# Optimization experiments

Measured on AMD Instinct MI355X. Metric: run time of the kernel, lower is better.

## Reference

```python
import jax, jax.numpy as jnp
import numpy as np

H, DK, D, DFF = 8, 64, 512, 512
B, S = 4, 1024
SCALE = 1.0 / np.sqrt(DK)


def _ln(x, g, b, eps=1e-5):
    m = jnp.mean(x, axis=-1, keepdims=True)
    v = jnp.mean((x - m) ** 2, axis=-1, keepdims=True)
    return (x - m) / jnp.sqrt(v + eps) * g + b


def _heads(x, w, b):
    bs, s, _ = x.shape
    return (x @ w + b).reshape(bs, s, H, DK).transpose(0, 2, 1, 3)  # [B,H,S,DK]


def _encoder_layer(x, qw, qb, kw, kb, vw, vb, ow, ob, g1, b1, w1, c1, w2, c2, g2, b2):
    # standard post-LN transformer encoder layer (sub_attention.Encoder(1))
    q = _heads(x, qw, qb)
    k = _heads(x, kw, kb)
    v = _heads(x, vw, vb)
    attn = jax.nn.softmax(jnp.einsum('bhqd,bhkd->bhqk', q, k) * SCALE, axis=-1)
    ctx = jnp.einsum('bhqk,bhkd->bhqd', attn, v).transpose(0, 2, 1, 3).reshape(x.shape[0], -1, H * DK)
    h = _ln(ctx @ ow + ob + x, g1, b1)
    f = jax.nn.relu(h @ w1 + c1) @ w2 + c2
    return _ln(f + h, g2, b2)


def setup_inputs() -> dict:
    key = jax.random.key(0)
    ks = iter(jax.random.split(key, 80))

    def nrm(*shape):
        return jax.random.normal(next(ks), shape, jnp.float32) * 0.02

    inp = {'audio_feat': jax.random.normal(next(ks), (B, S, D), jnp.float32),
           'video_feat': jax.random.normal(next(ks), (B, S, D), jnp.float32)}
    for p in ['aq', 'ak', 'av', 'vq', 'vk', 'vv', 'out']:
        inp[p + '_w'] = nrm(D, D)
        inp[p + '_b'] = jnp.zeros((D,), jnp.float32)
    inp['ln_g'] = jnp.ones((D,), jnp.float32)
    inp['ln_b'] = jnp.zeros((D,), jnp.float32)
    for pfx in ['asa_', 'vsa_']:
        for wn in ['qw', 'kw', 'vw', 'ow']:
            inp[pfx + wn] = nrm(D, D)
        for bn in ['qb', 'kb', 'vb', 'ob']:
            inp[pfx + bn] = jnp.zeros((D,), jnp.float32)
        inp[pfx + 'w1'] = nrm(D, DFF)
        inp[pfx + 'c1'] = jnp.zeros((DFF,), jnp.float32)
        inp[pfx + 'w2'] = nrm(DFF, D)
        inp[pfx + 'c2'] = jnp.zeros((D,), jnp.float32)
        inp[pfx + 'g1'] = jnp.ones((D,), jnp.float32)
        inp[pfx + 'b1'] = jnp.zeros((D,), jnp.float32)
        inp[pfx + 'g2'] = jnp.ones((D,), jnp.float32)
        inp[pfx + 'b2'] = jnp.zeros((D,), jnp.float32)
    return inp


def reference(audio_feat, video_feat, aq_w, aq_b, ak_w, ak_b, av_w, av_b, vq_w, vq_b, vk_w, vk_b, vv_w, vv_b, out_w, out_b, ln_g, ln_b, asa_qw, asa_qb, asa_kw, asa_kb, asa_vw, asa_vb, asa_ow, asa_ob, asa_g1, asa_b1, asa_w1, asa_c1, asa_w2, asa_c2, asa_g2, asa_b2, vsa_qw, vsa_qb, vsa_kw, vsa_kb, vsa_vw, vsa_vb, vsa_ow, vsa_ob, vsa_g1, vsa_b1, vsa_w1, vsa_c1, vsa_w2, vsa_c2, vsa_g2, vsa_b2):
    audio_self = _encoder_layer(audio_feat, asa_qw, asa_qb, asa_kw, asa_kb, asa_vw, asa_vb, asa_ow, asa_ob, asa_g1, asa_b1, asa_w1, asa_c1, asa_w2, asa_c2, asa_g2, asa_b2)
    video_self = _encoder_layer(video_feat, vsa_qw, vsa_qb, vsa_kw, vsa_kb, vsa_vw, vsa_vb, vsa_ow, vsa_ob, vsa_g1, vsa_b1, vsa_w1, vsa_c1, vsa_w2, vsa_c2, vsa_g2, vsa_b2)
    qa = _heads(audio_feat, aq_w, aq_b)
    ka = _heads(audio_feat, ak_w, ak_b)
    va = _heads(audio_feat, av_w, av_b)
    qv = _heads(video_feat, vq_w, vq_b)
    kv = _heads(video_feat, vk_w, vk_b)
    vvh = _heads(video_feat, vv_w, vv_b)
    attn_a = jax.nn.softmax(jnp.einsum('bhqd,bhkd->bhqk', qa, ka) * SCALE, axis=-1)
    attn_v = jax.nn.softmax(jnp.einsum('bhqd,bhkd->bhqk', qv, kv) * SCALE, axis=-1)
    attn = attn_a * attn_v  # dual-softmax elementwise combine
    ctx = jnp.einsum('bhqk,bhkd->bhqd', attn, va) * jnp.einsum('bhqk,bhkd->bhqd', attn, vvh)
    ctx = ctx.transpose(0, 2, 1, 3).reshape(audio_feat.shape[0], -1, H * DK)
    context = ctx @ out_w + out_b
    return _ln(audio_feat + context + audio_self + video_self, ln_g, ln_b)
```

## Files before the change

kernel.cpp:

```cpp
#include <hip/hip_runtime.h>
#include <cstddef>
#include <cstdint>


typedef __attribute__((ext_vector_type(8))) short s8v;
typedef __attribute__((ext_vector_type(4))) short s4v;
typedef __attribute__((ext_vector_type(4))) float f4v;

#define QSC 0.1803368801111444f
#define EXP2(x) __builtin_amdgcn_exp2f(x)
#define WAITV(N) asm volatile("s_waitcnt vmcnt(" #N ")" ::: "memory")
#define BAR() __builtin_amdgcn_s_barrier()

static __device__ __forceinline__ short f2bf(float f){
  unsigned int u = __builtin_bit_cast(unsigned int, f);
  u += 0x7fffu + ((u >> 16) & 1u);
  return (short)(u >> 16);
}
static __device__ __forceinline__ float bf2f(short s){
  unsigned int u = ((unsigned int)(unsigned short)s) << 16;
  return __builtin_bit_cast(float, u);
}
static __device__ __forceinline__ void gload16(const void* g, void* l){
  __builtin_amdgcn_global_load_lds(
      (const __attribute__((address_space(1))) unsigned int*)g,
      (__attribute__((address_space(3))) unsigned int*)l, 16, 0, 0);
}
#define MFMA16(a,b,c) __builtin_amdgcn_mfma_f32_16x16x32_bf16(a,b,c,0,0,0)

__global__ __launch_bounds__(256) void convert_in(const float* __restrict__ a,
                                                  const float* __restrict__ v,
                                                  short* __restrict__ oa,
                                                  short* __restrict__ ov){
  const float* src = blockIdx.y ? v : a;
  short* dst = blockIdx.y ? ov : oa;
  const int i = (blockIdx.x * 256 + threadIdx.x) * 8;
  float4 x = *reinterpret_cast<const float4*>(src + i);
  float4 y = *reinterpret_cast<const float4*>(src + i + 4);
  s8v o;
  o[0]=f2bf(x.x); o[1]=f2bf(x.y); o[2]=f2bf(x.z); o[3]=f2bf(x.w);
  o[4]=f2bf(y.x); o[5]=f2bf(y.y); o[6]=f2bf(y.z); o[7]=f2bf(y.w);
  *reinterpret_cast<s8v*>(dst + i) = o;
}

struct Ptr19 { const float* p[19]; };
__global__ __launch_bounds__(256) void pack_w(Ptr19 ws, short* __restrict__ wp){
  const int mat = blockIdx.y;
  const float* W = ws.p[mat];
  const int f = blockIdx.x * 256 + threadIdx.x;
  const int nblk = f >> 10, kg = (f >> 4) & 63, nl = f & 15;
  const int n = nblk * 16 + nl, k = kg * 8;
  s8v o;
#pragma unroll
  for (int e = 0; e < 8; ++e) o[e] = f2bf(W[(size_t)(k + e) * 512 + n]);
  *reinterpret_cast<s8v*>(wp + (size_t)mat * 262144 + (size_t)f * 8) = o;
}

struct GemmJobs { const short* A[12]; const short* W[12]; const float* bias[12];
                  short* C[12]; int mode[12]; };

template<bool RELU>
__global__ __launch_bounds__(256) void gemm_bf16(GemmJobs J){
  int i = (blockIdx.z * 32 + blockIdx.y) * 4 + blockIdx.x;
  const int c = (128 * gridDim.z) >> 3;
  i = (i & 7) * c + (i >> 3);
  const int z = i >> 7, rem = i & 127;
  const int by = rem >> 2, bx = rem & 3;

  const short* __restrict__ A = J.A[z];
  const short* __restrict__ Wp = J.W[z];
  const float* __restrict__ bias = J.bias[z];
  short* __restrict__ C = J.C[z];
  const int md = J.mode[z];
  __shared__ short As[2][4096], Bs[2][4096];
  const int tid = threadIdx.x, lane = tid & 63, w = tid >> 6;
  const int wm = w >> 1, wn = w & 1;
  const int m0 = by * 128, n0 = bx * 128;
  const int lh = lane >> 4, ll = lane & 15;
  f4v acc[4][4] = {};

  auto stage = [&](int kt, int buf){
    const int k0 = kt * 32;
#pragma unroll
    for (int p = 0; p < 2; ++p){
      const int f = tid + 256 * p;
      const int blk = f >> 6, kg = (f >> 4) & 3, il = f & 15;
      gload16(A + (size_t)(m0 + blk * 16 + il) * 512 + k0 + kg * 8, &As[buf][f * 8]);
      gload16(Wp + ((size_t)(((n0 >> 4) + blk) * 64 + (k0 >> 3) + kg) * 16 + il) * 8,
              &Bs[buf][f * 8]);
    }
  };

  stage(0, 0);
#pragma unroll
  for (int kt = 0; kt < 16; ++kt){
    if (kt < 15) { stage(kt + 1, (kt + 1) & 1); WAITV(4); }
    else         { WAITV(0); }
    BAR();
    const int cur = kt & 1;
    s8v a[4], b[4];
#pragma unroll
    for (int q = 0; q < 4; ++q)
      a[q] = *reinterpret_cast<const s8v*>(&As[cur][(((wm*4+q)*4 + lh)*16 + ll) * 8]);
#pragma unroll
    for (int j = 0; j < 4; ++j)
      b[j] = *reinterpret_cast<const s8v*>(&Bs[cur][(((wn*4+j)*4 + lh)*16 + ll) * 8]);
#pragma unroll
    for (int q = 0; q < 4; ++q)
#pragma unroll
      for (int j = 0; j < 4; ++j)
        acc[q][j] = MFMA16(a[q], b[j], acc[q][j]);
    BAR();
  }

  if (md == 2){
#pragma unroll
    for (int j = 0; j < 4; ++j){
      const int col = n0 + wn * 64 + j * 16 + ll;
      const float bv = bias[col];
      const int hh = col >> 6, dl = col & 63, dblk = dl >> 4, il = dl & 15;
#pragma unroll
      for (int q = 0; q < 4; ++q){
        const int rowb = m0 + wm * 64 + q * 16 + lh * 4;
        const int bb = rowb >> 10, srow = rowb & 1023;
        const size_t off = ((size_t)((bb*8 + hh)*16 + (srow >> 6))) * 4096
                         + (size_t)(((dblk << 7) + (((srow >> 3) & 7) << 4) + il) * 8 + (srow & 7));
        s4v o4;
#pragma unroll
        for (int r = 0; r < 4; ++r) o4[r] = f2bf(acc[q][j][r] + bv);
        *reinterpret_cast<s4v*>(&C[off]) = o4;
      }
    }
  } else {
    short* epi = (w < 2) ? &As[w][0] : &Bs[w - 2][0];
    const float sc = (md == 1) ? QSC : 1.0f;
#pragma unroll
    for (int j = 0; j < 4; ++j){
      const float bv = bias[n0 + wn * 64 + j * 16 + ll];
#pragma unroll
      for (int q = 0; q < 4; ++q)
#pragma unroll
        for (int r = 0; r < 4; ++r){
          float v = (acc[q][j][r] + bv) * sc;
          if (RELU) v = fmaxf(v, 0.f);
          epi[(q*16 + lh*4 + r)*64 + j*16 + ll] = f2bf(v);
        }
    }
#pragma unroll
    for (int i2 = 0; i2 < 8; ++i2){
      const int row = i2 * 8 + (lane >> 3);
      s8v vr = *reinterpret_cast<const s8v*>(&epi[row*64 + (lane & 7)*8]);
      *reinterpret_cast<s8v*>(&C[(size_t)(m0 + wm*64 + row)*512 + n0 + wn*64 + (lane&7)*8]) = vr;
    }
  }
}

template<bool RELU>
__global__ __launch_bounds__(256) void gemm_n64(GemmJobs J){
  int i = (blockIdx.z * 32 + blockIdx.y) * 8 + blockIdx.x;
  const int c = (256 * gridDim.z) >> 3;
  i = (i & 7) * c + (i >> 3);
  const int z = i >> 8, rem = i & 255;
  const int by = rem >> 3, bx = rem & 7;

  const short* __restrict__ A = J.A[z];
  const short* __restrict__ Wp = J.W[z];
  const float* __restrict__ bias = J.bias[z];
  short* __restrict__ C = J.C[z];
  __shared__ short As[2][4096], Bs[2][2048];
  const int tid = threadIdx.x, lane = tid & 63, w = tid >> 6;
  const int wm = w >> 1, wn = w & 1;
  const int m0 = by * 128, n0 = bx * 64;
  const int lh = lane >> 4, ll = lane & 15;
  f4v acc[4][2] = {};

  auto stage = [&](int kt, int buf){
    const int k0 = kt * 32;
#pragma unroll
    for (int p = 0; p < 2; ++p){
      const int f = tid + 256 * p;
      const int blk = f >> 6, kg = (f >> 4) & 3, il = f & 15;
      gload16(A + (size_t)(m0 + blk * 16 + il) * 512 + k0 + kg * 8, &As[buf][f * 8]);
    }
    {
      const int f = tid;
      const int blk = f >> 6, kg = (f >> 4) & 3, il = f & 15;
      gload16(Wp + ((size_t)(((n0 >> 4) + blk) * 64 + (k0 >> 3) + kg) * 16 + il) * 8,
              &Bs[buf][f * 8]);
    }
  };

  stage(0, 0);
#pragma unroll
  for (int kt = 0; kt < 16; ++kt){
    if (kt < 15) { stage(kt + 1, (kt + 1) & 1); WAITV(3); }
    else         { WAITV(0); }
    BAR();
    const int cur = kt & 1;
    s8v a[4], b[2];
#pragma unroll
    for (int q = 0; q < 4; ++q)
      a[q] = *reinterpret_cast<const s8v*>(&As[cur][(((wm*4+q)*4 + lh)*16 + ll) * 8]);
#pragma unroll
    for (int j = 0; j < 2; ++j)
      b[j] = *reinterpret_cast<const s8v*>(&Bs[cur][(((wn*2+j)*4 + lh)*16 + ll) * 8]);
#pragma unroll
    for (int q = 0; q < 4; ++q)
#pragma unroll
      for (int j = 0; j < 2; ++j)
        acc[q][j] = MFMA16(a[q], b[j], acc[q][j]);
    BAR();
  }

  short* epi = &As[0][0] + w * 2048;
#pragma unroll
  for (int j = 0; j < 2; ++j){
    const float bv = bias[n0 + wn * 32 + j * 16 + ll];
#pragma unroll
    for (int q = 0; q < 4; ++q)
#pragma unroll
      for (int r = 0; r < 4; ++r){
        float v = acc[q][j][r] + bv;
        if (RELU) v = fmaxf(v, 0.f);
        epi[(q*16 + lh*4 + r)*32 + j*16 + ll] = f2bf(v);
      }
  }
#pragma unroll
  for (int i2 = 0; i2 < 4; ++i2){
    const int row = i2 * 16 + (lane >> 2);
    s8v vr = *reinterpret_cast<const s8v*>(&epi[row*32 + (lane & 3)*8]);
    *reinterpret_cast<s8v*>(&C[(size_t)(m0 + wm*64 + row)*512 + n0 + wn*32 + (lane&3)*8]) = vr;
  }
}

struct AttnJob { const short* Q; const short* K; const short* Vp; short* O; };

__global__ __launch_bounds__(512) void attn_enc(AttnJob j0, AttnJob j1){
  const AttnJob jb = blockIdx.z ? j1 : j0;
  __shared__ short KT[2][4096], VT[2][4096];
  __shared__ short PL[8][1024];
  const int tid = threadIdx.x, lane = tid & 63, w = tid >> 6;
  int bi = blockIdx.y * 8 + blockIdx.x;
  bi = (bi & 7) * 32 + (bi >> 3);
  const int qt = bi & 7, bh = bi >> 3;
  const int b = bh >> 3, h = bh & 7;
  const int q0 = qt * 128;
  const size_t base = (size_t)b * 1024 * 512 + (size_t)h * 64;
  const int lh = lane >> 4, ll = lane & 15;
  short* PLw = PL[w];

  s8v qf[2];
#pragma unroll
  for (int df = 0; df < 2; ++df)
    qf[df] = *reinterpret_cast<const s8v*>(jb.Q + base + (size_t)(q0 + w*16 + ll)*512 + lh*8 + df*32);

  const int sblk = tid >> 7, sg8 = (tid >> 4) & 7, sil = tid & 15;
  auto stage = [&](int it, int buf){
    gload16(jb.K + base + (size_t)(it*64 + sblk*16 + sil)*512 + sg8*8, &KT[buf][tid*8]);
    gload16(jb.Vp + ((size_t)bh*16 + it)*4096 + (size_t)tid*8, &VT[buf][tid*8]);
  };

  f4v o[4] = {};
  float lp[4] = {0.f, 0.f, 0.f, 0.f};

  stage(0, 0);
#pragma unroll 1
  for (int it = 0; it < 16; ++it){
    if (it < 15) { stage(it + 1, (it + 1) & 1); WAITV(2); }
    else         { WAITV(0); }
    BAR();
    const int cur = it & 1;

    f4v s[4] = {};
#pragma unroll
    for (int fn = 0; fn < 4; ++fn)
#pragma unroll
      for (int df = 0; df < 2; ++df){
        s8v kf = *reinterpret_cast<const s8v*>(&KT[cur][((fn*8 + lh + df*4)*16 + ll) * 8]);
        s[fn] = MFMA16(qf[df], kf, s[fn]);
      }

    float px[4][4];
#pragma unroll
    for (int r = 0; r < 4; ++r){
      float p0 = EXP2(s[0][r]), p1 = EXP2(s[1][r]);
      float p2 = EXP2(s[2][r]), p3 = EXP2(s[3][r]);
      px[r][0]=p0; px[r][1]=p1; px[r][2]=p2; px[r][3]=p3;
      lp[r] += (p0 + p1) + (p2 + p3);
    }
#pragma unroll
    for (int r = 0; r < 4; ++r)
#pragma unroll
      for (int fn = 0; fn < 4; ++fn){
        const int q = lh*4 + r, k = fn*16 + ll, kg = k >> 3;
        PLw[(kg*16 + (q ^ kg))*8 + (k & 7)] = f2bf(px[r][fn]);
      }
    s8v pa[2];
#pragma unroll
    for (int kf2 = 0; kf2 < 2; ++kf2){
      const int kg = lh + kf2*4;
      pa[kf2] = *reinterpret_cast<const s8v*>(&PLw[(kg*16 + (ll ^ kg))*8]);
    }
#pragma unroll
    for (int fd = 0; fd < 4; ++fd)
#pragma unroll
      for (int kf2 = 0; kf2 < 2; ++kf2){
        s8v vf = *reinterpret_cast<const s8v*>(&VT[cur][((fd*8 + lh + kf2*4)*16 + ll) * 8]);
        o[fd] = MFMA16(pa[kf2], vf, o[fd]);
      }
    BAR();
  }

#pragma unroll
  for (int r = 0; r < 4; ++r){
    float Z = lp[r];
    Z += __shfl_xor(Z, 1); Z += __shfl_xor(Z, 2);
    Z += __shfl_xor(Z, 4); Z += __shfl_xor(Z, 8);
    const float rz = 1.f / Z;
#pragma unroll
    for (int fd = 0; fd < 4; ++fd)
      jb.O[base + (size_t)(q0 + w*16 + lh*4 + r)*512 + fd*16 + ll] = f2bf(o[fd][r] * rz);
  }
}

__global__ __launch_bounds__(512) void attn_dual(const short* __restrict__ Qa, const short* __restrict__ Ka,
                                                 const short* __restrict__ Vap, const short* __restrict__ Qv,
                                                 const short* __restrict__ Kv, const short* __restrict__ Vvp,
                                                 short* __restrict__ O){
  __shared__ short KTa[2][4096], KTv[2][4096], VTa[2][4096], VTv[2][4096];
  __shared__ short PL[8][1024];
  const int tid = threadIdx.x, lane = tid & 63, w = tid >> 6;
  int bi = blockIdx.y * 8 + blockIdx.x;
  bi = (bi & 7) * 32 + (bi >> 3);
  const int qt = bi & 7, bh = bi >> 3;
  const int b = bh >> 3, h = bh & 7;
  const int q0 = qt * 128;
  const size_t base = (size_t)b * 1024 * 512 + (size_t)h * 64;
  const int lh = lane >> 4, ll = lane & 15;
  short* PLw = PL[w];

  s8v qfa[2], qfv[2];
#pragma unroll
  for (int df = 0; df < 2; ++df){
    const size_t ro = base + (size_t)(q0 + w*16 + ll)*512 + lh*8 + df*32;
    qfa[df] = *reinterpret_cast<const s8v*>(Qa + ro);
    qfv[df] = *reinterpret_cast<const s8v*>(Qv + ro);
  }

  const int sblk = tid >> 7, sg8 = (tid >> 4) & 7, sil = tid & 15;
  auto stage = [&](int it, int buf){
    const size_t krow = base + (size_t)(it*64 + sblk*16 + sil)*512 + sg8*8;
    gload16(Ka + krow, &KTa[buf][tid*8]);
    gload16(Kv + krow, &KTv[buf][tid*8]);
    const size_t voff = ((size_t)bh*16 + it)*4096 + (size_t)tid*8;
    gload16(Vap + voff, &VTa[buf][tid*8]);
    gload16(Vvp + voff, &VTv[buf][tid*8]);
  };

  f4v oa[4] = {}, ov[4] = {};
  float lap[4] = {0,0,0,0}, lvp[4] = {0,0,0,0};

  stage(0, 0);
#pragma unroll 1
  for (int it = 0; it < 16; ++it){
    if (it < 15) { stage(it + 1, (it + 1) & 1); WAITV(4); }
    else         { WAITV(0); }
    BAR();
    const int cur = it & 1;

    f4v sa[4] = {}, sv[4] = {};
#pragma unroll
    for (int fn = 0; fn < 4; ++fn)
#pragma unroll
      for (int df = 0; df < 2; ++df){
        const int boff = ((fn*8 + lh + df*4)*16 + ll) * 8;
        s8v ka = *reinterpret_cast<const s8v*>(&KTa[cur][boff]);
        s8v kv = *reinterpret_cast<const s8v*>(&KTv[cur][boff]);
        sa[fn] = MFMA16(qfa[df], ka, sa[fn]);
        sv[fn] = MFMA16(qfv[df], kv, sv[fn]);
      }

    float pt[4][4];
#pragma unroll
    for (int r = 0; r < 4; ++r){
      float a0 = EXP2(sa[0][r]), a1 = EXP2(sa[1][r]);
      float a2 = EXP2(sa[2][r]), a3 = EXP2(sa[3][r]);
      float v0 = EXP2(sv[0][r]), v1 = EXP2(sv[1][r]);
      float v2 = EXP2(sv[2][r]), v3 = EXP2(sv[3][r]);
      lap[r] += (a0 + a1) + (a2 + a3);
      lvp[r] += (v0 + v1) + (v2 + v3);
      pt[r][0] = a0*v0; pt[r][1] = a1*v1; pt[r][2] = a2*v2; pt[r][3] = a3*v3;
    }
#pragma unroll
    for (int r = 0; r < 4; ++r)
#pragma unroll
      for (int fn = 0; fn < 4; ++fn){
        const int q = lh*4 + r, k = fn*16 + ll, kg = k >> 3;
        PLw[(kg*16 + (q ^ kg))*8 + (k & 7)] = f2bf(pt[r][fn]);
      }
    s8v pa[2];
#pragma unroll
    for (int kf2 = 0; kf2 < 2; ++kf2){
      const int kg = lh + kf2*4;
      pa[kf2] = *reinterpret_cast<const s8v*>(&PLw[(kg*16 + (ll ^ kg))*8]);
    }
#pragma unroll
    for (int fd = 0; fd < 4; ++fd)
#pragma unroll
      for (int kf2 = 0; kf2 < 2; ++kf2){
        const int boff = ((fd*8 + lh + kf2*4)*16 + ll) * 8;
        s8v va = *reinterpret_cast<const s8v*>(&VTa[cur][boff]);
        s8v vv = *reinterpret_cast<const s8v*>(&VTv[cur][boff]);
        oa[fd] = MFMA16(pa[kf2], va, oa[fd]);
        ov[fd] = MFMA16(pa[kf2], vv, ov[fd]);
      }
    BAR();
  }

#pragma unroll
  for (int r = 0; r < 4; ++r){
    float Za = lap[r], Zv = lvp[r];
    Za += __shfl_xor(Za, 1); Za += __shfl_xor(Za, 2);
    Za += __shfl_xor(Za, 4); Za += __shfl_xor(Za, 8);
    Zv += __shfl_xor(Zv, 1); Zv += __shfl_xor(Zv, 2);
    Zv += __shfl_xor(Zv, 4); Zv += __shfl_xor(Zv, 8);
    const float rz = 1.f / (Za * Zv);
#pragma unroll
    for (int fd = 0; fd < 4; ++fd){
      const float v = (oa[fd][r] * rz) * (ov[fd][r] * rz);
      O[base + (size_t)(q0 + w*16 + lh*4 + r)*512 + fd*16 + ll] = f2bf(v);
    }
  }
}

struct LnJob { const short* xb0; const short* xb1; const short* xb2;
               const float* xf; const float* g; const float* bb; void* out; };

template<int NBF, bool ADDF32, bool OUTF32>
__global__ __launch_bounds__(256) void ln_fused(LnJob j0, LnJob j1){
  const LnJob j = blockIdx.y ? j1 : j0;
  const int row = blockIdx.x, t = threadIdx.x;
  const size_t base = (size_t)row * 512;
  float x[2];
#pragma unroll
  for (int u = 0; u < 2; ++u){
    const int c = t + u * 256;
    float v = bf2f(j.xb0[base + c]);
    if (NBF > 1) v += bf2f(j.xb1[base + c]);
    if (NBF > 2) v += bf2f(j.xb2[base + c]);
    if (ADDF32) v += j.xf[base + c];
    x[u] = v;
  }
  float s = x[0] + x[1], ss = x[0]*x[0] + x[1]*x[1];
#pragma unroll
  for (int o = 32; o; o >>= 1){ s += __shfl_xor(s, o); ss += __shfl_xor(ss, o); }
  __shared__ float rb[8];
  const int wv = t >> 6;
  if ((t & 63) == 0){ rb[wv] = s; rb[wv + 4] = ss; }
  __syncthreads();
  s  = rb[0] + rb[1] + rb[2] + rb[3];
  ss = rb[4] + rb[5] + rb[6] + rb[7];
  const float m = s * (1.f / 512.f);
  const float var = ss * (1.f / 512.f) - m * m;
  const float rstd = rsqrtf(var + 1e-5f);
#pragma unroll
  for (int u = 0; u < 2; ++u){
    const int c = t + u * 256;
    const float v = (x[u] - m) * rstd * j.g[c] + j.bb[c];
    if (OUTF32) ((float*)j.out)[base + c] = v;
    else        ((short*)j.out)[base + c] = f2bf(v);
  }
}

__global__ __launch_bounds__(256) void ln_final(const short* __restrict__ fa, const short* __restrict__ ha,
                                                const short* __restrict__ fv, const short* __restrict__ hv,
                                                const short* __restrict__ ctx, const float* __restrict__ audio,
                                                const float* __restrict__ g2a, const float* __restrict__ b2a,
                                                const float* __restrict__ g2v, const float* __restrict__ b2v,
                                                const float* __restrict__ gf, const float* __restrict__ bf,
                                                float* __restrict__ out){
  const int row = blockIdx.x, t = threadIdx.x;
  const size_t base = (size_t)row * 512;
  __shared__ float rb[24];
  const int wv = t >> 6;

  auto reduce2 = [&](float a, float b, int p){
    float s = a + b, ss = a*a + b*b;
#pragma unroll
    for (int o = 32; o; o >>= 1){ s += __shfl_xor(s, o); ss += __shfl_xor(ss, o); }
    if ((t & 63) == 0){ rb[p*8 + wv] = s; rb[p*8 + 4 + wv] = ss; }
  };
  auto stats = [&](int p, float& m, float& rstd){
    const float s  = rb[p*8+0] + rb[p*8+1] + rb[p*8+2] + rb[p*8+3];
    const float ss = rb[p*8+4] + rb[p*8+5] + rb[p*8+6] + rb[p*8+7];
    m = s * (1.f / 512.f);
    rstd = rsqrtf(ss * (1.f / 512.f) - m * m + 1e-5f);
  };

  float xa[2], xv[2];
#pragma unroll
  for (int u = 0; u < 2; ++u){
    const int c = t + u * 256;
    xa[u] = bf2f(fa[base + c]) + bf2f(ha[base + c]);
    xv[u] = bf2f(fv[base + c]) + bf2f(hv[base + c]);
  }
  reduce2(xa[0], xa[1], 0);
  reduce2(xv[0], xv[1], 1);
  __syncthreads();
  float ma, ra, mv, rv;
  stats(0, ma, ra);
  stats(1, mv, rv);

  float xf[2];
#pragma unroll
  for (int u = 0; u < 2; ++u){
    const int c = t + u * 256;
    const float sa = (xa[u] - ma) * ra * g2a[c] + b2a[c];
    const float sv = (xv[u] - mv) * rv * g2v[c] + b2v[c];
    xf[u] = audio[base + c] + bf2f(ctx[base + c]) + sa + sv;
  }
  reduce2(xf[0], xf[1], 2);
  __syncthreads();
  float mf, rf;
  stats(2, mf, rf);
#pragma unroll
  for (int u = 0; u < 2; ++u){
    const int c = t + u * 256;
    out[base + c] = (xf[u] - mf) * rf * gf[c] + bf[c];
  }
}

extern "C" void kernel_launch(void* const* d_in, const int* in_sizes, int n_in,
                              void* d_out, int out_size, void* d_ws, size_t ws_size,
                              hipStream_t stream) {
  const float* audio = (const float*)d_in[0];
  const float* video = (const float*)d_in[1];
  auto F = [&](int i){ return (const float*)d_in[i]; };

  short* ws16 = (short*)d_ws;
  const size_t SL = 2097152;
  auto S = [&](int i){ return ws16 + (size_t)i * SL; };
  short* Wp = S(12);
  auto WP = [&](int i){ return (const short*)(Wp + (size_t)i * 262144); };
  short* Kcv = (short*)d_out;
  short* Vcv = (short*)d_out + SL;

  convert_in<<<dim3(1024,2), 256, 0, stream>>>(audio, video, S(10), S(11));

  Ptr19 pw;
  const int widx[19] = {18,19,20,21,26,28, 34,35,36,37,42,44, 2,4,6,8,10,12, 14};
  for (int i = 0; i < 19; ++i) pw.p[i] = F(widx[i]);
  pack_w<<<dim3(128,19), 256, 0, stream>>>(pw, Wp);

  GemmJobs g1{};
  const short* g1A[12] = {S(10),S(10),S(10), S(11),S(11),S(11), S(10),S(10),S(10), S(11),S(11),S(11)};
  const short* g1W[12] = {WP(0),WP(1),WP(2), WP(6),WP(7),WP(8), WP(12),WP(13),WP(14), WP(15),WP(16),WP(17)};
  const float* g1B[12] = {F(22),F(23),F(24), F(38),F(39),F(40), F(3),F(5),F(7), F(9),F(11),F(13)};
  short*       g1C[12] = {S(0),S(1),S(2), S(3),S(4),S(5), S(6),S(7),S(8), S(9),Kcv,Vcv};
  const int    g1M[12] = {1,0,2, 1,0,2, 1,0,2, 1,0,2};
  for (int i = 0; i < 12; ++i){ g1.A[i]=g1A[i]; g1.W[i]=g1W[i]; g1.bias[i]=g1B[i]; g1.C[i]=g1C[i]; g1.mode[i]=g1M[i]; }
  gemm_bf16<false><<<dim3(4,32,12), 256, 0, stream>>>(g1);

  attn_enc<<<dim3(8,32,2), 512, 0, stream>>>(AttnJob{S(0),S(1),S(2),S(10)},
                                             AttnJob{S(3),S(4),S(5),S(11)});

  attn_dual<<<dim3(8,32), 512, 0, stream>>>(S(6),S(7),S(8), S(9),Kcv,Vcv, S(0));

  GemmJobs g39{};
  g39.A[0]=S(10); g39.W[0]=WP(3);  g39.bias[0]=F(25); g39.C[0]=S(1); g39.mode[0]=0;
  g39.A[1]=S(11); g39.W[1]=WP(9);  g39.bias[1]=F(41); g39.C[1]=S(2); g39.mode[1]=0;
  g39.A[2]=S(0);  g39.W[2]=WP(18); g39.bias[2]=F(15); g39.C[2]=S(3); g39.mode[2]=0;
  gemm_n64<false><<<dim3(8,32,3), 256, 0, stream>>>(g39);

  ln_fused<1,true,false><<<dim3(4096,2), 256, 0, stream>>>(
      LnJob{S(1),nullptr,nullptr, audio, F(30),F(31), S(4)},
      LnJob{S(2),nullptr,nullptr, video, F(46),F(47), S(5)});

  GemmJobs g5{};
  g5.A[0]=S(4); g5.W[0]=WP(4);  g5.bias[0]=F(27); g5.C[0]=S(6); g5.mode[0]=0;
  g5.A[1]=S(5); g5.W[1]=WP(10); g5.bias[1]=F(43); g5.C[1]=S(7); g5.mode[1]=0;
  gemm_n64<true><<<dim3(8,32,2), 256, 0, stream>>>(g5);

  GemmJobs g6{};
  g6.A[0]=S(6); g6.W[0]=WP(5);  g6.bias[0]=F(29); g6.C[0]=S(8); g6.mode[0]=0;
  g6.A[1]=S(7); g6.W[1]=WP(11); g6.bias[1]=F(45); g6.C[1]=S(9); g6.mode[1]=0;
  gemm_n64<false><<<dim3(8,32,2), 256, 0, stream>>>(g6);

  ln_final<<<4096, 256, 0, stream>>>(S(8),S(4), S(9),S(5), S(3), audio,
                                     F(32),F(33), F(48),F(49), F(16),F(17),
                                     (float*)d_out);
}
```

Baseline: 183.0 us.

## Halve attention block threads so each wave computes two query tiles

Both attention kernels now run 4 waves per block instead of 8. Each wave handles 32 query rows as two 16-row tiles, so every K and V fragment read from shared memory feeds two MFMAs. Staging is split into two load passes per thread and the vmcnt waits are doubled to match. The aim is fewer LDS reads per MFMA and cheaper barriers, at the cost of higher register pressure and fewer waves available to hide latency.

```diff
diff --git a/kernel.cpp b/kernel.cpp
--- a/kernel.cpp
+++ b/kernel.cpp
@@ -235,10 +235,10 @@
 
 struct AttnJob { const short* Q; const short* K; const short* Vp; short* O; };
 
-__global__ __launch_bounds__(512) void attn_enc(AttnJob j0, AttnJob j1){
+__global__ __launch_bounds__(256) void attn_enc(AttnJob j0, AttnJob j1){
   const AttnJob jb = blockIdx.z ? j1 : j0;
   __shared__ short KT[2][4096], VT[2][4096];
-  __shared__ short PL[8][1024];
+  __shared__ short PL[4][2048];
   const int tid = threadIdx.x, lane = tid & 63, w = tid >> 6;
   int bi = blockIdx.y * 8 + blockIdx.x;
   bi = (bi & 7) * 32 + (bi >> 3);
@@ -247,88 +247,107 @@
   const int q0 = qt * 128;
   const size_t base = (size_t)b * 1024 * 512 + (size_t)h * 64;
   const int lh = lane >> 4, ll = lane & 15;
-  short* PLw = PL[w];
-
-  s8v qf[2];
-#pragma unroll
-  for (int df = 0; df < 2; ++df)
-    qf[df] = *reinterpret_cast<const s8v*>(jb.Q + base + (size_t)(q0 + w*16 + ll)*512 + lh*8 + df*32);
-
-  const int sblk = tid >> 7, sg8 = (tid >> 4) & 7, sil = tid & 15;
+
+  s8v qf[2][2];
+#pragma unroll
+  for (int t = 0; t < 2; ++t)
+#pragma unroll
+    for (int df = 0; df < 2; ++df)
+      qf[t][df] = *reinterpret_cast<const s8v*>(
+          jb.Q + base + (size_t)(q0 + w*32 + t*16 + ll)*512 + lh*8 + df*32);
+
   auto stage = [&](int it, int buf){
-    gload16(jb.K + base + (size_t)(it*64 + sblk*16 + sil)*512 + sg8*8, &KT[buf][tid*8]);
-    gload16(jb.Vp + ((size_t)bh*16 + it)*4096 + (size_t)tid*8, &VT[buf][tid*8]);
+#pragma unroll
+    for (int p = 0; p < 2; ++p){
+      const int f = tid + 256 * p;
+      const int sblk = f >> 7, sg8 = (f >> 4) & 7, sil = f & 15;
+      gload16(jb.K + base + (size_t)(it*64 + sblk*16 + sil)*512 + sg8*8, &KT[buf][f*8]);
+      gload16(jb.Vp + ((size_t)bh*16 + it)*4096 + (size_t)f*8, &VT[buf][f*8]);
+    }
   };
 
-  f4v o[4] = {};
-  float lp[4] = {0.f, 0.f, 0.f, 0.f};
+  f4v o[2][4] = {};
+  float lp[2][4] = {};
 
   stage(0, 0);
 #pragma unroll 1
   for (int it = 0; it < 16; ++it){
-    if (it < 15) { stage(it + 1, (it + 1) & 1); WAITV(2); }
+    if (it < 15) { stage(it + 1, (it + 1) & 1); WAITV(4); }
     else         { WAITV(0); }
     BAR();
     const int cur = it & 1;
 
-    f4v s[4] = {};
+    f4v s[2][4] = {};
 #pragma unroll
     for (int fn = 0; fn < 4; ++fn)
 #pragma unroll
       for (int df = 0; df < 2; ++df){
         s8v kf = *reinterpret_cast<const s8v*>(&KT[cur][((fn*8 + lh + df*4)*16 + ll) * 8]);
-        s[fn] = MFMA16(qf[df], kf, s[fn]);
-      }
-
-    float px[4][4];
-#pragma unroll
-    for (int r = 0; r < 4; ++r){
-      float p0 = EXP2(s[0][r]), p1 = EXP2(s[1][r]);
-      float p2 = EXP2(s[2][r]), p3 = EXP2(s[3][r]);
-      px[r][0]=p0; px[r][1]=p1; px[r][2]=p2; px[r][3]=p3;
-      lp[r] += (p0 + p1) + (p2 + p3);
-    }
-#pragma unroll
-    for (int r = 0; r < 4; ++r)
-#pragma unroll
-      for (int fn = 0; fn < 4; ++fn){
-        const int q = lh*4 + r, k = fn*16 + ll, kg = k >> 3;
-        PLw[(kg*16 + (q ^ kg))*8 + (k & 7)] = f2bf(px[r][fn]);
-      }
-    s8v pa[2];
-#pragma unroll
-    for (int kf2 = 0; kf2 < 2; ++kf2){
-      const int kg = lh + kf2*4;
-      pa[kf2] = *reinterpret_cast<const s8v*>(&PLw[(kg*16 + (ll ^ kg))*8]);
-    }
+#pragma unroll
+        for (int t = 0; t < 2; ++t)
+          s[t][fn] = MFMA16(qf[t][df], kf, s[t][fn]);
+      }
+
+#pragma unroll
+    for (int t = 0; t < 2; ++t){
+      short* PLt = &PL[w][t*1024];
+      float px[4][4];
+#pragma unroll
+      for (int r = 0; r < 4; ++r){
+        float p0 = EXP2(s[t][0][r]), p1 = EXP2(s[t][1][r]);
+        float p2 = EXP2(s[t][2][r]), p3 = EXP2(s[t][3][r]);
+        px[r][0]=p0; px[r][1]=p1; px[r][2]=p2; px[r][3]=p3;
+        lp[t][r] += (p0 + p1) + (p2 + p3);
+      }
+#pragma unroll
+      for (int r = 0; r < 4; ++r)
+#pragma unroll
+        for (int fn = 0; fn < 4; ++fn){
+          const int q = lh*4 + r, k = fn*16 + ll, kg = k >> 3;
+          PLt[(kg*16 + (q ^ kg))*8 + (k & 7)] = f2bf(px[r][fn]);
+        }
+    }
+    s8v pa[2][2];
+#pragma unroll
+    for (int t = 0; t < 2; ++t)
+#pragma unroll
+      for (int kf2 = 0; kf2 < 2; ++kf2){
+        const int kg = lh + kf2*4;
+        pa[t][kf2] = *reinterpret_cast<const s8v*>(&PL[w][t*1024 + (kg*16 + (ll ^ kg))*8]);
+      }
 #pragma unroll
     for (int fd = 0; fd < 4; ++fd)
 #pragma unroll
       for (int kf2 = 0; kf2 < 2; ++kf2){
         s8v vf = *reinterpret_cast<const s8v*>(&VT[cur][((fd*8 + lh + kf2*4)*16 + ll) * 8]);
-        o[fd] = MFMA16(pa[kf2], vf, o[fd]);
-      }
-    BAR();
-  }
-
-#pragma unroll
-  for (int r = 0; r < 4; ++r){
-    float Z = lp[r];
-    Z += __shfl_xor(Z, 1); Z += __shfl_xor(Z, 2);
-    Z += __shfl_xor(Z, 4); Z += __shfl_xor(Z, 8);
-    const float rz = 1.f / Z;
-#pragma unroll
-    for (int fd = 0; fd < 4; ++fd)
-      jb.O[base + (size_t)(q0 + w*16 + lh*4 + r)*512 + fd*16 + ll] = f2bf(o[fd][r] * rz);
-  }
-}
-
-__global__ __launch_bounds__(512) void attn_dual(const short* __restrict__ Qa, const short* __restrict__ Ka,
+#pragma unroll
+        for (int t = 0; t < 2; ++t)
+          o[t][fd] = MFMA16(pa[t][kf2], vf, o[t][fd]);
+      }
+    BAR();
+  }
+
+#pragma unroll
+  for (int t = 0; t < 2; ++t)
+#pragma unroll
+    for (int r = 0; r < 4; ++r){
+      float Z = lp[t][r];
+      Z += __shfl_xor(Z, 1); Z += __shfl_xor(Z, 2);
+      Z += __shfl_xor(Z, 4); Z += __shfl_xor(Z, 8);
+      const float rz = 1.f / Z;
+#pragma unroll
+      for (int fd = 0; fd < 4; ++fd)
+        jb.O[base + (size_t)(q0 + w*32 + t*16 + lh*4 + r)*512 + fd*16 + ll]
+            = f2bf(o[t][fd][r] * rz);
+    }
+}
+
+__global__ __launch_bounds__(256) void attn_dual(const short* __restrict__ Qa, const short* __restrict__ Ka,
                                                  const short* __restrict__ Vap, const short* __restrict__ Qv,
                                                  const short* __restrict__ Kv, const short* __restrict__ Vvp,
                                                  short* __restrict__ O){
   __shared__ short KTa[2][4096], KTv[2][4096], VTa[2][4096], VTv[2][4096];
-  __shared__ short PL[8][1024];
+  __shared__ short PL[4][2048];
   const int tid = threadIdx.x, lane = tid & 63, w = tid >> 6;
   int bi = blockIdx.y * 8 + blockIdx.x;
   bi = (bi & 7) * 32 + (bi >> 3);
@@ -337,38 +356,43 @@
   const int q0 = qt * 128;
   const size_t base = (size_t)b * 1024 * 512 + (size_t)h * 64;
   const int lh = lane >> 4, ll = lane & 15;
-  short* PLw = PL[w];
-
-  s8v qfa[2], qfv[2];
-#pragma unroll
-  for (int df = 0; df < 2; ++df){
-    const size_t ro = base + (size_t)(q0 + w*16 + ll)*512 + lh*8 + df*32;
-    qfa[df] = *reinterpret_cast<const s8v*>(Qa + ro);
-    qfv[df] = *reinterpret_cast<const s8v*>(Qv + ro);
-  }
-
-  const int sblk = tid >> 7, sg8 = (tid >> 4) & 7, sil = tid & 15;
+
+  s8v qfa[2][2], qfv[2][2];
+#pragma unroll
+  for (int t = 0; t < 2; ++t)
+#pragma unroll
+    for (int df = 0; df < 2; ++df){
+      const size_t ro = base + (size_t)(q0 + w*32 + t*16 + ll)*512 + lh*8 + df*32;
+      qfa[t][df] = *reinterpret_cast<const s8v*>(Qa + ro);
+      qfv[t][df] = *reinterpret_cast<const s8v*>(Qv + ro);
+    }
+
   auto stage = [&](int it, int buf){
-    const size_t krow = base + (size_t)(it*64 + sblk*16 + sil)*512 + sg8*8;
-    gload16(Ka + krow, &KTa[buf][tid*8]);
-    gload16(Kv + krow, &KTv[buf][tid*8]);
-    const size_t voff = ((size_t)bh*16 + it)*4096 + (size_t)tid*8;
-    gload16(Vap + voff, &VTa[buf][tid*8]);
-    gload16(Vvp + voff, &VTv[buf][tid*8]);
+#pragma unroll
+    for (int p = 0; p < 2; ++p){
+      const int f = tid + 256 * p;
+      const int sblk = f >> 7, sg8 = (f >> 4) & 7, sil = f & 15;
+      const size_t krow = base + (size_t)(it*64 + sblk*16 + sil)*512 + sg8*8;
+      gload16(Ka + krow, &KTa[buf][f*8]);
+      gload16(Kv + krow, &KTv[buf][f*8]);
+      const size_t voff = ((size_t)bh*16 + it)*4096 + (size_t)f*8;
+      gload16(Vap + voff, &VTa[buf][f*8]);
+      gload16(Vvp + voff, &VTv[buf][f*8]);
+    }
   };
 
-  f4v oa[4] = {}, ov[4] = {};
-  float lap[4] = {0,0,0,0}, lvp[4] = {0,0,0,0};
+  f4v oa[2][4] = {}, ov[2][4] = {};
+  float lap[2][4] = {}, lvp[2][4] = {};
 
   stage(0, 0);
 #pragma unroll 1
   for (int it = 0; it < 16; ++it){
-    if (it < 15) { stage(it + 1, (it + 1) & 1); WAITV(4); }
+    if (it < 15) { stage(it + 1, (it + 1) & 1); WAITV(8); }
     else         { WAITV(0); }
     BAR();
     const int cur = it & 1;
 
-    f4v sa[4] = {}, sv[4] = {};
+    f4v sa[2][4] = {}, sv[2][4] = {};
 #pragma unroll
     for (int fn = 0; fn < 4; ++fn)
 #pragma unroll
@@ -376,34 +400,43 @@
         const int boff = ((fn*8 + lh + df*4)*16 + ll) * 8;
         s8v ka = *reinterpret_cast<const s8v*>(&KTa[cur][boff]);
         s8v kv = *reinterpret_cast<const s8v*>(&KTv[cur][boff]);
-        sa[fn] = MFMA16(qfa[df], ka, sa[fn]);
-        sv[fn] = MFMA16(qfv[df], kv, sv[fn]);
-      }
-
-    float pt[4][4];
-#pragma unroll
-    for (int r = 0; r < 4; ++r){
-      float a0 = EXP2(sa[0][r]), a1 = EXP2(sa[1][r]);
-      float a2 = EXP2(sa[2][r]), a3 = EXP2(sa[3][r]);
-      float v0 = EXP2(sv[0][r]), v1 = EXP2(sv[1][r]);
-      float v2 = EXP2(sv[2][r]), v3 = EXP2(sv[3][r]);
-      lap[r] += (a0 + a1) + (a2 + a3);
-      lvp[r] += (v0 + v1) + (v2 + v3);
-      pt[r][0] = a0*v0; pt[r][1] = a1*v1; pt[r][2] = a2*v2; pt[r][3] = a3*v3;
-    }
-#pragma unroll
-    for (int r = 0; r < 4; ++r)
-#pragma unroll
-      for (int fn = 0; fn < 4; ++fn){
-        const int q = lh*4 + r, k = fn*16 + ll, kg = k >> 3;
-        PLw[(kg*16 + (q ^ kg))*8 + (k & 7)] = f2bf(pt[r][fn]);
-      }
-    s8v pa[2];
-#pragma unroll
-    for (int kf2 = 0; kf2 < 2; ++kf2){
-      const int kg = lh + kf2*4;
-      pa[kf2] = *reinterpret_cast<const s8v*>(&PLw[(kg*16 + (ll ^ kg))*8]);
-    }
+#pragma unroll
+        for (int t = 0; t < 2; ++t){
+          sa[t][fn] = MFMA16(qfa[t][df], ka, sa[t][fn]);
+          sv[t][fn] = MFMA16(qfv[t][df], kv, sv[t][fn]);
+        }
+      }
+
+#pragma unroll
+    for (int t = 0; t < 2; ++t){
+      short* PLt = &PL[w][t*1024];
+      float pt[4][4];
+#pragma unroll
+      for (int r = 0; r < 4; ++r){
+        float a0 = EXP2(sa[t][0][r]), a1 = EXP2(sa[t][1][r]);
+        float a2 = EXP2(sa[t][2][r]), a3 = EXP2(sa[t][3][r]);
+        float v0 = EXP2(sv[t][0][r]), v1 = EXP2(sv[t][1][r]);
+        float v2 = EXP2(sv[t][2][r]), v3 = EXP2(sv[t][3][r]);
+        lap[t][r] += (a0 + a1) + (a2 + a3);
+        lvp[t][r] += (v0 + v1) + (v2 + v3);
+        pt[r][0] = a0*v0; pt[r][1] = a1*v1; pt[r][2] = a2*v2; pt[r][3] = a3*v3;
+      }
+#pragma unroll
+      for (int r = 0; r < 4; ++r)
+#pragma unroll
+        for (int fn = 0; fn < 4; ++fn){
+          const int q = lh*4 + r, k = fn*16 + ll, kg = k >> 3;
+          PLt[(kg*16 + (q ^ kg))*8 + (k & 7)] = f2bf(pt[r][fn]);
+        }
+    }
+    s8v pa[2][2];
+#pragma unroll
+    for (int t = 0; t < 2; ++t)
+#pragma unroll
+      for (int kf2 = 0; kf2 < 2; ++kf2){
+        const int kg = lh + kf2*4;
+        pa[t][kf2] = *reinterpret_cast<const s8v*>(&PL[w][t*1024 + (kg*16 + (ll ^ kg))*8]);
+      }
 #pragma unroll
     for (int fd = 0; fd < 4; ++fd)
 #pragma unroll
@@ -411,26 +444,31 @@
         const int boff = ((fd*8 + lh + kf2*4)*16 + ll) * 8;
         s8v va = *reinterpret_cast<const s8v*>(&VTa[cur][boff]);
         s8v vv = *reinterpret_cast<const s8v*>(&VTv[cur][boff]);
-        oa[fd] = MFMA16(pa[kf2], va, oa[fd]);
-        ov[fd] = MFMA16(pa[kf2], vv, ov[fd]);
-      }
-    BAR();
-  }
-
-#pragma unroll
-  for (int r = 0; r < 4; ++r){
-    float Za = lap[r], Zv = lvp[r];
-    Za += __shfl_xor(Za, 1); Za += __shfl_xor(Za, 2);
-    Za += __shfl_xor(Za, 4); Za += __shfl_xor(Za, 8);
-    Zv += __shfl_xor(Zv, 1); Zv += __shfl_xor(Zv, 2);
-    Zv += __shfl_xor(Zv, 4); Zv += __shfl_xor(Zv, 8);
-    const float rz = 1.f / (Za * Zv);
-#pragma unroll
-    for (int fd = 0; fd < 4; ++fd){
-      const float v = (oa[fd][r] * rz) * (ov[fd][r] * rz);
-      O[base + (size_t)(q0 + w*16 + lh*4 + r)*512 + fd*16 + ll] = f2bf(v);
-    }
-  }
+#pragma unroll
+        for (int t = 0; t < 2; ++t){
+          oa[t][fd] = MFMA16(pa[t][kf2], va, oa[t][fd]);
+          ov[t][fd] = MFMA16(pa[t][kf2], vv, ov[t][fd]);
+        }
+      }
+    BAR();
+  }
+
+#pragma unroll
+  for (int t = 0; t < 2; ++t)
+#pragma unroll
+    for (int r = 0; r < 4; ++r){
+      float Za = lap[t][r], Zv = lvp[t][r];
+      Za += __shfl_xor(Za, 1); Za += __shfl_xor(Za, 2);
+      Za += __shfl_xor(Za, 4); Za += __shfl_xor(Za, 8);
+      Zv += __shfl_xor(Zv, 1); Zv += __shfl_xor(Zv, 2);
+      Zv += __shfl_xor(Zv, 4); Zv += __shfl_xor(Zv, 8);
+      const float rz = 1.f / (Za * Zv);
+#pragma unroll
+      for (int fd = 0; fd < 4; ++fd){
+        const float v = (oa[t][fd][r] * rz) * (ov[t][fd][r] * rz);
+        O[base + (size_t)(q0 + w*32 + t*16 + lh*4 + r)*512 + fd*16 + ll] = f2bf(v);
+      }
+    }
 }
 
 struct LnJob { const short* xb0; const short* xb1; const short* xb2;
@@ -561,10 +599,10 @@
   for (int i = 0; i < 12; ++i){ g1.A[i]=g1A[i]; g1.W[i]=g1W[i]; g1.bias[i]=g1B[i]; g1.C[i]=g1C[i]; g1.mode[i]=g1M[i]; }
   gemm_bf16<false><<<dim3(4,32,12), 256, 0, stream>>>(g1);
 
-  attn_enc<<<dim3(8,32,2), 512, 0, stream>>>(AttnJob{S(0),S(1),S(2),S(10)},
+  attn_enc<<<dim3(8,32,2), 256, 0, stream>>>(AttnJob{S(0),S(1),S(2),S(10)},
                                              AttnJob{S(3),S(4),S(5),S(11)});
 
-  attn_dual<<<dim3(8,32), 512, 0, stream>>>(S(6),S(7),S(8), S(9),Kcv,Vcv, S(0));
+  attn_dual<<<dim3(8,32), 256, 0, stream>>>(S(6),S(7),S(8), S(9),Kcv,Vcv, S(0));
 
   GemmJobs g39{};
   g39.A[0]=S(10); g39.W[0]=WP(3);  g39.bias[0]=F(25); g39.C[0]=S(1); g39.mode[0]=0;
```

Measured after the change: 197.7 us. 1.08x slower.
